# Kernel tuning notes

Measured on AMD Instinct MI355X. Metric: run time of the kernel, lower is better.

## Reference

```python
import jax, jax.numpy as jnp
import numpy as np

B, T, C, H = 2, 2048, 1024, 16
D = C // H  # head dim = 64
EPS = 1e-5


def layernorm(x, g, b):
    mu = jnp.mean(x, axis=-1, keepdims=True)
    var = jnp.var(x, axis=-1, keepdims=True)
    return (x - mu) * jax.lax.rsqrt(var + EPS) * g + b


def setup_inputs() -> dict:
    key = jax.random.key(0)
    ks = jax.random.split(key, 8)
    init_scale = 0.25
    return {
        "x": jax.random.normal(ks[0], (B, T, C), dtype=jnp.float32),
        # weights stored [in, out] (transpose of torch Linear)
        "w_qkv": jax.random.normal(ks[1], (C, 3 * C), dtype=jnp.float32) * init_scale,
        "b_qkv": jnp.zeros((3 * C,), dtype=jnp.float32),
        "w_proj": jax.random.normal(ks[2], (C, C), dtype=jnp.float32) * init_scale,
        "b_proj": jnp.zeros((C,), dtype=jnp.float32),
        "ln1_g": jnp.ones((C,), dtype=jnp.float32),
        "ln1_b": jnp.zeros((C,), dtype=jnp.float32),
        "w_fc": jax.random.normal(ks[3], (C, 4 * C), dtype=jnp.float32) * init_scale,
        "b_fc": jnp.zeros((4 * C,), dtype=jnp.float32),
        "w_out": jax.random.normal(ks[4], (4 * C, C), dtype=jnp.float32) * init_scale,
        "b_out": jnp.zeros((C,), dtype=jnp.float32),
        "ln2_g": jnp.ones((C,), dtype=jnp.float32),
        "ln2_b": jnp.zeros((C,), dtype=jnp.float32),
    }


def reference(x, w_qkv, b_qkv, w_proj, b_proj, ln1_g, ln1_b,
              w_fc, b_fc, w_out, b_out, ln2_g, ln2_b):
    # ---- attention sub-block (pre-LN) ----
    h = layernorm(x, ln1_g, ln1_b)
    qkv = h @ w_qkv + b_qkv                      # [B,T,3C]
    q, k, v = jnp.split(qkv, 3, axis=-1)
    q = q.reshape(B, T, H, D)
    k = k.reshape(B, T, H, D)
    v = v.reshape(B, T, H, D)
    scores = jnp.einsum('bthd,bshd->bhts', q, k) * (1.0 / np.sqrt(D))
    attn = jax.nn.softmax(scores, axis=-1)       # full [B,H,T,T] as in source
    out = jnp.einsum('bhts,bshd->bthd', attn, v).reshape(B, T, C)
    x = x + out @ w_proj + b_proj
    # ---- MLP sub-block (pre-LN) ----
    h = layernorm(x, ln2_g, ln2_b)
    h = jax.nn.gelu(h @ w_fc + b_fc, approximate=False)  # torch nn.GELU default = exact
    x = x + h @ w_out + b_out
    return x
```

## Files before the change

### kernel.cpp

```cpp
#include <hip/hip_runtime.h>
#include <hip/hip_bf16.h>
#include <math.h>

#define DEVINL static __device__ __forceinline__

typedef _Float16 f16x8 __attribute__((ext_vector_type(8)));
typedef _Float16 f16x4 __attribute__((ext_vector_type(4)));
typedef float f32x4 __attribute__((ext_vector_type(4)));
typedef float f32x16 __attribute__((ext_vector_type(16)));

constexpr int TT = 2048, CC = 1024, HH = 16, DD = 64;
constexpr int HALF_Y = 2 * TT * CC;
constexpr int HALF_L = 2 * HH * TT;

DEVINL void gload_lds16(const void* g, void* s) {
  __builtin_amdgcn_global_load_lds(
      (const __attribute__((address_space(1))) void*)g,
      (__attribute__((address_space(3))) void*)s, 16, 0, 0);
}

DEVINL unsigned pkrtz(float a, float b) {
  typedef __fp16 hf2 __attribute__((ext_vector_type(2)));
  union { hf2 h; unsigned u; } c;
  c.h = __builtin_amdgcn_cvt_pkrtz(a, b);
  return c.u;
}

DEVINL float fast_gelu(float v) {
  float z = v * (2.302208214f + 0.102945116f * v * v);
  return v * __builtin_amdgcn_rcpf(1.0f + exp2f(-z));
}

__global__ __launch_bounds__(256) void transpose_cast(
    const float* __restrict__ in, _Float16* __restrict__ out, int K, int N) {
  __shared__ float tile[32][33];
  int n0 = blockIdx.x * 32, k0 = blockIdx.y * 32;
  int tx = threadIdx.x & 31, ty = threadIdx.x >> 5;
  #pragma unroll
  for (int i = 0; i < 32; i += 8)
    tile[ty + i][tx] = in[(size_t)(k0 + ty + i) * N + n0 + tx];
  __syncthreads();
  #pragma unroll
  for (int i = 0; i < 32; i += 8)
    out[(size_t)(n0 + ty + i) * K + k0 + tx] = (_Float16)tile[tx][ty + i];
}

__global__ __launch_bounds__(256) void ln_cast(
    const float* __restrict__ x, const float* __restrict__ g,
    const float* __restrict__ bta, _Float16* __restrict__ out) {
  int row = blockIdx.x, t = threadIdx.x;
  float4 v = ((const float4*)(x + (size_t)row * CC))[t];
  float s = v.x + v.y + v.z + v.w;
  float s2 = v.x * v.x + v.y * v.y + v.z * v.z + v.w * v.w;
  #pragma unroll
  for (int o = 32; o >= 1; o >>= 1) { s += __shfl_xor(s, o); s2 += __shfl_xor(s2, o); }
  __shared__ float ss[4], ssq[4];
  int w = t >> 6;
  if ((t & 63) == 0) { ss[w] = s; ssq[w] = s2; }
  __syncthreads();
  s = ss[0] + ss[1] + ss[2] + ss[3];
  s2 = ssq[0] + ssq[1] + ssq[2] + ssq[3];
  float mu = s * (1.0f / CC);
  float rs = rsqrtf(s2 * (1.0f / CC) - mu * mu + 1e-5f);
  float4 gv = ((const float4*)g)[t];
  float4 bv = ((const float4*)bta)[t];
  f16x4 o4;
  o4[0] = (_Float16)((v.x - mu) * rs * gv.x + bv.x);
  o4[1] = (_Float16)((v.y - mu) * rs * gv.y + bv.y);
  o4[2] = (_Float16)((v.z - mu) * rs * gv.z + bv.z);
  o4[3] = (_Float16)((v.w - mu) * rs * gv.w + bv.w);
  ((f16x4*)(out + (size_t)row * CC))[t] = o4;
}

template <int EPI, int N, int K, int BN, int DBUF>
__global__ __launch_bounds__(256) void gemm_bt(
    const _Float16* __restrict__ A, const _Float16* __restrict__ Bt,
    const float* __restrict__ bias, const float* __restrict__ res,
    void* __restrict__ outp) {
  constexpr int NWN = BN / 64;
  constexpr int MI = 2 * NWN;
  constexpr int NB = DBUF ? 2 : 1;
  constexpr int NLOADS = 4 + BN / 32;
  __shared__ __align__(16) _Float16 As[NB][128 * 64];
  __shared__ __align__(16) _Float16 Bs[NB][BN * 64];
  const int bm0 = blockIdx.y * 128, bn0 = blockIdx.x * BN;
  const int t = threadIdx.x, w = t >> 6, l = t & 63, lg = l >> 4, lr = l & 15;
  const int wr = w / NWN, wc = w % NWN;
  const int srow = t >> 3, sc = t & 7;
  f32x4 acc[MI][4] = {};

  auto STAGE = [&](int bi, int k0) {
    #pragma unroll
    for (int q = 0; q < 4; ++q) {
      int row = q * 32 + srow;
      int gc = sc ^ (row & 7);
      gload_lds16(A + (size_t)(bm0 + row) * K + k0 + gc * 8, As[bi] + row * 64 + sc * 8);
    }
    #pragma unroll
    for (int q = 0; q < BN / 32; ++q) {
      int row = q * 32 + srow;
      int gc = sc ^ (row & 7);
      gload_lds16(Bt + (size_t)(bn0 + row) * K + k0 + gc * 8, Bs[bi] + row * 64 + sc * 8);
    }
  };
  auto COMPUTE = [&](const _Float16* Ac, const _Float16* Bc) {
    #pragma unroll
    for (int ks = 0; ks < 2; ++ks) {
      f16x8 af[MI], bfr[4];
      #pragma unroll
      for (int mi = 0; mi < MI; ++mi) {
        int row = wr * (16 * MI) + mi * 16 + lr;
        af[mi] = *(const f16x8*)(Ac + row * 64 + (((ks * 4 + lg) ^ (row & 7)) << 3));
      }
      #pragma unroll
      for (int ni = 0; ni < 4; ++ni) {
        int row = wc * 64 + ni * 16 + lr;
        bfr[ni] = *(const f16x8*)(Bc + row * 64 + (((ks * 4 + lg) ^ (row & 7)) << 3));
      }
      #pragma unroll
      for (int mi = 0; mi < MI; ++mi)
        #pragma unroll
        for (int ni = 0; ni < 4; ++ni)
          acc[mi][ni] = __builtin_amdgcn_mfma_f32_16x16x32_f16(af[mi], bfr[ni], acc[mi][ni], 0, 0, 0);
    }
  };

  if constexpr (DBUF) {
    STAGE(0, 0);
    int cur = 0;
    for (int k0 = 0; k0 < K; k0 += 64) {
      if (k0 + 64 < K) {
        STAGE(cur ^ 1, k0 + 64);
        asm volatile("s_waitcnt vmcnt(%0)" :: "i"(NLOADS) : "memory");
      } else {
        asm volatile("s_waitcnt vmcnt(0)" ::: "memory");
      }
      __builtin_amdgcn_s_barrier();
      COMPUTE(As[cur], Bs[cur]);
      __builtin_amdgcn_s_barrier();
      cur ^= 1;
    }
  } else {
    for (int k0 = 0; k0 < K; k0 += 64) {
      STAGE(0, k0);
      __syncthreads();
      COMPUTE(As[0], Bs[0]);
      __syncthreads();
    }
  }

  #pragma unroll
  for (int mi = 0; mi < MI; ++mi) {
    #pragma unroll
    for (int ni = 0; ni < 4; ++ni) {
      int gc = bn0 + wc * 64 + ni * 16 + lr;
      float bv = bias[gc];
      #pragma unroll
      for (int r = 0; r < 4; ++r) {
        int gr = bm0 + wr * (16 * MI) + mi * 16 + lg * 4 + r;
        float v = acc[mi][ni][r] + bv;
        if constexpr (EPI == 1) {
          ((_Float16*)outp)[(size_t)gr * N + gc] = (_Float16)fast_gelu(v);
        } else {
          ((float*)outp)[(size_t)gr * N + gc] = res[(size_t)gr * N + gc] + v;
        }
      }
    }
  }
}

__global__ __launch_bounds__(256) void gemm_qkv(
    const _Float16* __restrict__ A, const _Float16* __restrict__ Bt,
    const float* __restrict__ bias,
    _Float16* __restrict__ qo, _Float16* __restrict__ ko,
    _Float16* __restrict__ vt) {
  __shared__ __align__(16) _Float16 As[128 * 64];
  __shared__ __align__(16) _Float16 Bs[128 * 64];
  const int bm0 = blockIdx.y * 128, bn0 = blockIdx.x * 128;
  const int t = threadIdx.x, w = t >> 6, l = t & 63, lg = l >> 4, lr = l & 15;
  const int wr = w >> 1, wc = w & 1;
  const int srow = t >> 3, sc = t & 7;
  f32x4 acc[4][4] = {};
  for (int k0 = 0; k0 < 1024; k0 += 64) {
    #pragma unroll
    for (int q = 0; q < 4; ++q) {
      int row = q * 32 + srow;
      int gc = sc ^ (row & 7);
      gload_lds16(A + (size_t)(bm0 + row) * 1024 + k0 + gc * 8, As + row * 64 + sc * 8);
      gload_lds16(Bt + (size_t)(bn0 + row) * 1024 + k0 + gc * 8, Bs + row * 64 + sc * 8);
    }
    __syncthreads();
    #pragma unroll
    for (int ks = 0; ks < 2; ++ks) {
      f16x8 af[4], bfr[4];
      #pragma unroll
      for (int mi = 0; mi < 4; ++mi) {
        int row = wr * 64 + mi * 16 + lr;
        af[mi] = *(const f16x8*)(As + row * 64 + (((ks * 4 + lg) ^ (row & 7)) << 3));
      }
      #pragma unroll
      for (int ni = 0; ni < 4; ++ni) {
        int row = wc * 64 + ni * 16 + lr;
        bfr[ni] = *(const f16x8*)(Bs + row * 64 + (((ks * 4 + lg) ^ (row & 7)) << 3));
      }
      #pragma unroll
      for (int mi = 0; mi < 4; ++mi)
        #pragma unroll
        for (int ni = 0; ni < 4; ++ni)
          acc[mi][ni] = __builtin_amdgcn_mfma_f32_16x16x32_f16(af[mi], bfr[ni], acc[mi][ni], 0, 0, 0);
    }
    __syncthreads();
  }
  const float QSCL = 0.125f * 1.44269504f;
  #pragma unroll
  for (int mi = 0; mi < 4; ++mi) {
    #pragma unroll
    for (int ni = 0; ni < 4; ++ni) {
      int gc = bn0 + wc * 64 + ni * 16 + lr;
      float bv = bias[gc];
      int sec = gc >> 10, cc = gc & 1023;
      #pragma unroll
      for (int r = 0; r < 4; ++r) {
        int gr = bm0 + wr * 64 + mi * 16 + lg * 4 + r;
        float v = acc[mi][ni][r] + bv;
        if (sec == 0) {
          qo[(size_t)gr * 1024 + cc] = (_Float16)(v * QSCL);
        } else if (sec == 1) {
          ko[(size_t)gr * 1024 + cc] = (_Float16)v;
        } else {
          int hh = cc >> 6, dd = cc & 63;
          int bb = gr >> 11, tk = gr & (TT - 1);
          vt[(((size_t)bb * HH + hh) * DD + dd) * TT + tk] = (_Float16)v;
        }
      }
    }
  }
}

__global__ __launch_bounds__(256, 4) void flash_attn(
    const _Float16* __restrict__ qg, const _Float16* __restrict__ kg,
    const _Float16* __restrict__ vt, _Float16* __restrict__ yp,
    float* __restrict__ Lp) {
  const int qt0 = blockIdx.x * 128, h = blockIdx.y;
  const int b = blockIdx.z & 1, half = blockIdx.z >> 1;
  const int kvbeg = half * (TT / 2), kvend = kvbeg + TT / 2;
  const int t = threadIdx.x, w = t >> 6, l = t & 63;
  const int l31 = l & 31, hi = l >> 5;
  __shared__ __align__(16) _Float16 Ks[2][64 * 64];
  __shared__ __align__(16) _Float16 VTs[2][64 * 64];
  const int srow = t >> 3, sc = t & 7;
  const int gc0 = sc ^ (srow & 7) ^ ((srow >> 3) & 7);
  const int gc1 = sc ^ (srow & 7) ^ (((srow >> 3) + 4) & 7);
  const _Float16* kg_r = kg + ((size_t)b * TT + srow) * CC + h * DD;
  const _Float16* vt_r = vt + (((size_t)b * HH + h) * DD + srow) * TT;
  const int dst0 = srow * 64 + sc * 8;

  f16x8 qf[4];
  {
    const _Float16* qp = qg + ((size_t)(b * TT + qt0 + w * 32 + l31)) * CC + h * DD + hi * 8;
    #pragma unroll
    for (int ks = 0; ks < 4; ++ks) qf[ks] = *(const f16x8*)(qp + ks * 16);
  }
  const int rx = l31 & 7, ry = (l31 >> 3) & 7;
  int swk[2], swv[2];
  #pragma unroll
  for (int sub = 0; sub < 2; ++sub) swk[sub] = rx ^ ((sub * 4 + ry) & 7);
  swv[0] = rx ^ ry;
  swv[1] = rx ^ ((4 + ry) & 7);

  f32x16 o0 = {}, o1 = {};
  float osum = 0.0f, mrow = -3.0e38f;

  auto STAGE = [&](int bufi, int kv0) {
    gload_lds16(kg_r + (size_t)kv0 * CC + gc0 * 8, Ks[bufi] + dst0);
    gload_lds16(kg_r + (size_t)(kv0 + 32) * CC + gc1 * 8, Ks[bufi] + 2048 + dst0);
    gload_lds16(vt_r + kv0 + gc0 * 8, VTs[bufi] + dst0);
    gload_lds16(vt_r + 32 * TT + kv0 + gc1 * 8, VTs[bufi] + 2048 + dst0);
  };
  STAGE(0, kvbeg);
  __syncthreads();
  int cur = 0;
  for (int kv0 = kvbeg; kv0 < kvend; kv0 += 64) {
    if (kv0 + 64 < kvend) STAGE(cur ^ 1, kv0 + 64);
    const _Float16* Kc = Ks[cur];
    const _Float16* Vc = VTs[cur];
    #pragma unroll
    for (int sub = 0; sub < 2; ++sub) {
      f32x16 s = {};
      const int krow = (sub * 32 + l31) * 64;
      __builtin_amdgcn_s_setprio(1);
      #pragma unroll
      for (int ks = 0; ks < 4; ++ks) {
        f16x8 kf = *(const f16x8*)(Kc + krow + (((ks * 2 + hi) ^ swk[sub]) << 3));
        s = __builtin_amdgcn_mfma_f32_32x32x16_f16(kf, qf[ks], s, 0, 0, 0);
      }
      __builtin_amdgcn_s_setprio(0);
      float m01 = fmaxf(fmaxf(s[0], s[1]), fmaxf(s[2], s[3]));
      float m23 = fmaxf(fmaxf(s[4], s[5]), fmaxf(s[6], s[7]));
      float m45 = fmaxf(fmaxf(s[8], s[9]), fmaxf(s[10], s[11]));
      float m67 = fmaxf(fmaxf(s[12], s[13]), fmaxf(s[14], s[15]));
      float m16v = fmaxf(fmaxf(m01, m23), fmaxf(m45, m67));
      int ok = (m16v <= mrow + 8.0f) ? 1 : 0;
      if (!__all(ok)) {
        float mo = fmaxf(m16v, __shfl_xor(m16v, 32));
        float mn = fmaxf(mrow, mo);
        float corr = exp2f(mrow - mn);
        mrow = mn;
        #pragma unroll
        for (int r = 0; r < 16; ++r) { o0[r] *= corr; o1[r] *= corr; }
        osum *= corr;
      }
      float p[16];
      float psum = 0.0f;
      #pragma unroll
      for (int r = 0; r < 16; ++r) { p[r] = exp2f(s[r] - mrow); psum += p[r]; }
      osum += psum;
      unsigned W[8], X[8];
      #pragma unroll
      for (int i = 0; i < 8; ++i) {
        W[i] = pkrtz(p[2 * i], p[2 * i + 1]);
        X[i] = __shfl_xor(W[i], 32);
      }
      union { unsigned u[4]; f16x8 v; } bp[2];
      #pragma unroll
      for (int s2 = 0; s2 < 2; ++s2) {
        bp[s2].u[0] = hi ? X[4 * s2 + 2] : W[4 * s2 + 0];
        bp[s2].u[1] = hi ? X[4 * s2 + 3] : W[4 * s2 + 1];
        bp[s2].u[2] = hi ? W[4 * s2 + 2] : X[4 * s2 + 0];
        bp[s2].u[3] = hi ? W[4 * s2 + 3] : X[4 * s2 + 1];
      }
      __builtin_amdgcn_s_setprio(1);
      #pragma unroll
      for (int s2 = 0; s2 < 2; ++s2) {
        int c = sub * 4 + s2 * 2 + hi;
        {
          f16x8 vf = *(const f16x8*)(Vc + l31 * 64 + ((c ^ swv[0]) << 3));
          o0 = __builtin_amdgcn_mfma_f32_32x32x16_f16(vf, bp[s2].v, o0, 0, 0, 0);
        }
        {
          f16x8 vf = *(const f16x8*)(Vc + (32 + l31) * 64 + ((c ^ swv[1]) << 3));
          o1 = __builtin_amdgcn_mfma_f32_32x32x16_f16(vf, bp[s2].v, o1, 0, 0, 0);
        }
      }
      __builtin_amdgcn_s_setprio(0);
    }
    __syncthreads();
    cur ^= 1;
  }
  osum += __shfl_xor(osum, 32);
  float rinv = 1.0f / osum;
  const int qrow = qt0 + w * 32 + l31;
  _Float16* ob = yp + (size_t)half * HALF_Y + ((size_t)(b * TT + qrow)) * CC + h * DD;
  #pragma unroll
  for (int i = 0; i < 4; ++i) {
    int col0 = 8 * i + 4 * hi;
    uint2 v0, v1;
    v0.x = pkrtz(o0[4 * i + 0] * rinv, o0[4 * i + 1] * rinv);
    v0.y = pkrtz(o0[4 * i + 2] * rinv, o0[4 * i + 3] * rinv);
    v1.x = pkrtz(o1[4 * i + 0] * rinv, o1[4 * i + 1] * rinv);
    v1.y = pkrtz(o1[4 * i + 2] * rinv, o1[4 * i + 3] * rinv);
    *(uint2*)(ob + col0) = v0;
    *(uint2*)(ob + 32 + col0) = v1;
  }
  if (hi == 0)
    Lp[(size_t)half * HALF_L + ((size_t)b * HH + h) * TT + qrow] =
        mrow + log2f(osum);
}

__global__ __launch_bounds__(256) void attn_combine(
    const _Float16* __restrict__ yp, const float* __restrict__ Lp,
    _Float16* __restrict__ att) {
  int bt = blockIdx.x;
  int b = bt >> 11, tt = bt & (TT - 1);
  int tid = threadIdx.x;
  int h = tid >> 4;
  size_t li = ((size_t)b * HH + h) * TT + tt;
  float L0 = Lp[li], L1 = Lp[HALF_L + li];
  float m = fmaxf(L0, L1);
  float w0 = exp2f(L0 - m), w1 = exp2f(L1 - m);
  float rs = 1.0f / (w0 + w1);
  w0 *= rs; w1 *= rs;
  f16x4 a = ((const f16x4*)(yp + (size_t)bt * CC))[tid];
  f16x4 c = ((const f16x4*)(yp + HALF_Y + (size_t)bt * CC))[tid];
  f16x4 o;
  #pragma unroll
  for (int i = 0; i < 4; ++i)
    o[i] = (_Float16)(w0 * (float)a[i] + w1 * (float)c[i]);
  ((f16x4*)(att + (size_t)bt * CC))[tid] = o;
}

extern "C" void kernel_launch(void* const* d_in, const int* in_sizes, int n_in,
                              void* d_out, int out_size, void* d_ws, size_t ws_size,
                              hipStream_t stream) {
  const float* x      = (const float*)d_in[0];
  const float* w_qkv  = (const float*)d_in[1];
  const float* b_qkv  = (const float*)d_in[2];
  const float* w_proj = (const float*)d_in[3];
  const float* b_proj = (const float*)d_in[4];
  const float* ln1_g  = (const float*)d_in[5];
  const float* ln1_b  = (const float*)d_in[6];
  const float* w_fc   = (const float*)d_in[7];
  const float* b_fc   = (const float*)d_in[8];
  const float* w_out  = (const float*)d_in[9];
  const float* b_out  = (const float*)d_in[10];
  const float* ln2_g  = (const float*)d_in[11];
  const float* ln2_b  = (const float*)d_in[12];

  char* ws = (char*)d_ws;
  _Float16* wqkv_t = (_Float16*)(ws);
  _Float16* wproj_t= (_Float16*)(ws + 6291456);
  _Float16* wfc_t  = (_Float16*)(ws + 8388608);
  _Float16* wout_t = (_Float16*)(ws + 16777216);
  _Float16* hslot  = (_Float16*)(ws + 25165824);
  _Float16* qbuf   = (_Float16*)(ws + 33554432);
  _Float16* kbuf   = (_Float16*)(ws + 41943040);
  _Float16* vtbuf  = (_Float16*)(ws + 50331648);
  _Float16* tbuf   = (_Float16*)(ws + 33554432);
  float*    x1     = (float*)(ws + 67108864);
  _Float16* ypart  = (_Float16*)(ws + 83886080);
  float*    Lpart  = (float*)(ws + 100663296);

  transpose_cast<<<dim3(96, 32), 256, 0, stream>>>(w_qkv, wqkv_t, 1024, 3072);
  transpose_cast<<<dim3(32, 32), 256, 0, stream>>>(w_proj, wproj_t, 1024, 1024);
  transpose_cast<<<dim3(128, 32), 256, 0, stream>>>(w_fc, wfc_t, 1024, 4096);
  transpose_cast<<<dim3(32, 128), 256, 0, stream>>>(w_out, wout_t, 4096, 1024);

  ln_cast<<<4096, 256, 0, stream>>>(x, ln1_g, ln1_b, hslot);
  gemm_qkv<<<dim3(24, 32), 256, 0, stream>>>(hslot, wqkv_t, b_qkv, qbuf, kbuf, vtbuf);
  flash_attn<<<dim3(16, 16, 4), 256, 0, stream>>>(qbuf, kbuf, vtbuf, ypart, Lpart);
  attn_combine<<<4096, 256, 0, stream>>>(ypart, Lpart, hslot);
  gemm_bt<2, 1024, 1024, 64, 1><<<dim3(16, 32), 256, 0, stream>>>(hslot, wproj_t, b_proj, x, x1);
  ln_cast<<<4096, 256, 0, stream>>>(x1, ln2_g, ln2_b, hslot);
  gemm_bt<1, 4096, 1024, 128, 0><<<dim3(32, 32), 256, 0, stream>>>(hslot, wfc_t, b_fc, nullptr, tbuf);
  gemm_bt<2, 1024, 4096, 64, 1><<<dim3(16, 32), 256, 0, stream>>>(tbuf, wout_t, b_out, x1, (float*)d_out);
}
```

Before: 286.0 us.

## Fuse weight transposes and first layernorm into one launch; XCD-swizzle GEMM tiles

Merges the four weight transpose-cast launches and the first layernorm into a single prep kernel that dispatches by block index, so fewer kernel launches and tail gaps occur. The GEMM kernels now use a flat 1D grid with an XCD-aware swizzle that places consecutive tiles on the same XCD, aiming for better L2 reuse of the A and B panels on MI355X. This adds divergent per-block branching in the prep kernel and ties tile mapping to grid sizes divisible by eight.

New measurement: 279.3 us. 1.02x faster.

```diff
diff --git a/kernel.cpp b/kernel.cpp
--- a/kernel.cpp
+++ b/kernel.cpp
@@ -31,11 +31,16 @@
   return v * __builtin_amdgcn_rcpf(1.0f + exp2f(-z));
 }
 
-__global__ __launch_bounds__(256) void transpose_cast(
-    const float* __restrict__ in, _Float16* __restrict__ out, int K, int N) {
+DEVINL int xcd_swizzle(int lid, int n) {
+  int cpx = n >> 3;
+  return (lid & 7) * cpx + (lid >> 3);
+}
+
+DEVINL void transpose_tile(const float* in, _Float16* out, int K, int N,
+                           int bx, int by, int tid) {
   __shared__ float tile[32][33];
-  int n0 = blockIdx.x * 32, k0 = blockIdx.y * 32;
-  int tx = threadIdx.x & 31, ty = threadIdx.x >> 5;
+  int n0 = bx * 32, k0 = by * 32;
+  int tx = tid & 31, ty = tid >> 5;
   #pragma unroll
   for (int i = 0; i < 32; i += 8)
     tile[ty + i][tx] = in[(size_t)(k0 + ty + i) * N + n0 + tx];
@@ -45,10 +50,8 @@
     out[(size_t)(n0 + ty + i) * K + k0 + tx] = (_Float16)tile[tx][ty + i];
 }
 
-__global__ __launch_bounds__(256) void ln_cast(
-    const float* __restrict__ x, const float* __restrict__ g,
-    const float* __restrict__ bta, _Float16* __restrict__ out) {
-  int row = blockIdx.x, t = threadIdx.x;
+DEVINL void ln_row(const float* x, const float* g, const float* bta,
+                   _Float16* out, int row, int t) {
   float4 v = ((const float4*)(x + (size_t)row * CC))[t];
   float s = v.x + v.y + v.z + v.w;
   float s2 = v.x * v.x + v.y * v.y + v.z * v.z + v.w * v.w;
@@ -72,18 +75,50 @@
   ((f16x4*)(out + (size_t)row * CC))[t] = o4;
 }
 
+__global__ __launch_bounds__(256) void prep_all(
+    const float* __restrict__ w_qkv, const float* __restrict__ w_proj,
+    const float* __restrict__ w_fc, const float* __restrict__ w_out,
+    const float* __restrict__ x, const float* __restrict__ ln1_g,
+    const float* __restrict__ ln1_b,
+    _Float16* __restrict__ wqkv_t, _Float16* __restrict__ wproj_t,
+    _Float16* __restrict__ wfc_t, _Float16* __restrict__ wout_t,
+    _Float16* __restrict__ h1) {
+  int lid = blockIdx.x, t = threadIdx.x;
+  if (lid < 3072) {
+    transpose_tile(w_qkv, wqkv_t, 1024, 3072, lid % 96, lid / 96, t);
+  } else if (lid < 4096) {
+    int l = lid - 3072;
+    transpose_tile(w_proj, wproj_t, 1024, 1024, l % 32, l / 32, t);
+  } else if (lid < 8192) {
+    int l = lid - 4096;
+    transpose_tile(w_fc, wfc_t, 1024, 4096, l % 128, l / 128, t);
+  } else if (lid < 12288) {
+    int l = lid - 8192;
+    transpose_tile(w_out, wout_t, 4096, 1024, l % 32, l / 32, t);
+  } else {
+    ln_row(x, ln1_g, ln1_b, h1, lid - 12288, t);
+  }
+}
+
+__global__ __launch_bounds__(256) void ln_cast(
+    const float* __restrict__ x, const float* __restrict__ g,
+    const float* __restrict__ bta, _Float16* __restrict__ out) {
+  ln_row(x, g, bta, out, blockIdx.x, threadIdx.x);
+}
+
 template <int EPI, int N, int K, int BN, int DBUF>
 __global__ __launch_bounds__(256) void gemm_bt(
     const _Float16* __restrict__ A, const _Float16* __restrict__ Bt,
     const float* __restrict__ bias, const float* __restrict__ res,
-    void* __restrict__ outp) {
+    void* __restrict__ outp, int nbx) {
   constexpr int NWN = BN / 64;
   constexpr int MI = 2 * NWN;
   constexpr int NB = DBUF ? 2 : 1;
   constexpr int NLOADS = 4 + BN / 32;
   __shared__ __align__(16) _Float16 As[NB][128 * 64];
   __shared__ __align__(16) _Float16 Bs[NB][BN * 64];
-  const int bm0 = blockIdx.y * 128, bn0 = blockIdx.x * BN;
+  const int swz = xcd_swizzle(blockIdx.x, gridDim.x);
+  const int bm0 = (swz / nbx) * 128, bn0 = (swz % nbx) * BN;
   const int t = threadIdx.x, w = t >> 6, l = t & 63, lg = l >> 4, lr = l & 15;
   const int wr = w / NWN, wc = w % NWN;
   const int srow = t >> 3, sc = t & 7;
@@ -176,7 +211,8 @@
     _Float16* __restrict__ vt) {
   __shared__ __align__(16) _Float16 As[128 * 64];
   __shared__ __align__(16) _Float16 Bs[128 * 64];
-  const int bm0 = blockIdx.y * 128, bn0 = blockIdx.x * 128;
+  const int swz = xcd_swizzle(blockIdx.x, gridDim.x);
+  const int bm0 = (swz / 24) * 128, bn0 = (swz % 24) * 128;
   const int t = threadIdx.x, w = t >> 6, l = t & 63, lg = l >> 4, lr = l & 15;
   const int wr = w >> 1, wc = w & 1;
   const int srow = t >> 3, sc = t & 7;
@@ -420,17 +456,13 @@
   _Float16* ypart  = (_Float16*)(ws + 83886080);
   float*    Lpart  = (float*)(ws + 100663296);
 
-  transpose_cast<<<dim3(96, 32), 256, 0, stream>>>(w_qkv, wqkv_t, 1024, 3072);
-  transpose_cast<<<dim3(32, 32), 256, 0, stream>>>(w_proj, wproj_t, 1024, 1024);
-  transpose_cast<<<dim3(128, 32), 256, 0, stream>>>(w_fc, wfc_t, 1024, 4096);
-  transpose_cast<<<dim3(32, 128), 256, 0, stream>>>(w_out, wout_t, 4096, 1024);
-
-  ln_cast<<<4096, 256, 0, stream>>>(x, ln1_g, ln1_b, hslot);
-  gemm_qkv<<<dim3(24, 32), 256, 0, stream>>>(hslot, wqkv_t, b_qkv, qbuf, kbuf, vtbuf);
+  prep_all<<<16384, 256, 0, stream>>>(w_qkv, w_proj, w_fc, w_out, x, ln1_g, ln1_b,
+                                      wqkv_t, wproj_t, wfc_t, wout_t, hslot);
+  gemm_qkv<<<768, 256, 0, stream>>>(hslot, wqkv_t, b_qkv, qbuf, kbuf, vtbuf);
   flash_attn<<<dim3(16, 16, 4), 256, 0, stream>>>(qbuf, kbuf, vtbuf, ypart, Lpart);
   attn_combine<<<4096, 256, 0, stream>>>(ypart, Lpart, hslot);
-  gemm_bt<2, 1024, 1024, 64, 1><<<dim3(16, 32), 256, 0, stream>>>(hslot, wproj_t, b_proj, x, x1);
+  gemm_bt<2, 1024, 1024, 64, 1><<<512, 256, 0, stream>>>(hslot, wproj_t, b_proj, x, x1, 16);
   ln_cast<<<4096, 256, 0, stream>>>(x1, ln2_g, ln2_b, hslot);
-  gemm_bt<1, 4096, 1024, 128, 0><<<dim3(32, 32), 256, 0, stream>>>(hslot, wfc_t, b_fc, nullptr, tbuf);
-  gemm_bt<2, 1024, 4096, 64, 1><<<dim3(16, 32), 256, 0, stream>>>(tbuf, wout_t, b_out, x1, (float*)d_out);
-}
+  gemm_bt<1, 4096, 1024, 128, 0><<<1024, 256, 0, stream>>>(hslot, wfc_t, b_fc, nullptr, tbuf, 32);
+  gemm_bt<2, 1024, 4096, 64, 1><<<512, 256, 0, stream>>>(tbuf, wout_t, b_out, x1, (float*)d_out, 16);
+}
```
